# Kernel optimization log

Hardware: AMD Instinct MI355X
Metric: run time of the kernel (lower is better)

Reference implementation:

```python
import jax, jax.numpy as jnp
import numpy as np

C = 16      # internal_channel
DG = 8      # deform groups
KK = 9      # 3x3 kernel


def conv2d(x, w, b, pad):
    out = jax.lax.conv_general_dilated(
        x, w, (1, 1), [(pad, pad), (pad, pad)],
        dimension_numbers=('NCHW', 'OIHW', 'NCHW'))
    return out + b[None, :, None, None]


def feature_extraction(img, w1, b1, w2, b2, w3, b3):
    f1 = jax.nn.relu(conv2d(img, w1, b1, 1))   # [B,C,H,W]
    f2 = jax.nn.relu(conv2d(f1, w2, b2, 0))    # [B,C,H-2,W-2]
    f3 = jax.nn.relu(conv2d(f2, w3, b3, 0))    # [B,C,H-4,W-4]
    return [f1, f2, f3]


def deform_conv(x, offset, w, b):
    # x: [B,C,H,W]; offset: [B, DG*KK*2, H, W] (y,x pairs); w: [Cout,C,3,3]
    B, Cin, H, W = x.shape
    Cg = Cin // DG
    off = offset.reshape(B, DG, KK, 2, H, W)
    ky = jnp.repeat(jnp.arange(3) - 1, 3)  # kernel y offsets (pad=1)
    kx = jnp.tile(jnp.arange(3) - 1, 3)
    base_y = jnp.arange(H).reshape(1, 1, 1, H, 1)
    base_x = jnp.arange(W).reshape(1, 1, 1, 1, W)
    sy = base_y + ky.reshape(1, 1, KK, 1, 1) + off[:, :, :, 0]  # [B,DG,KK,H,W]
    sx = base_x + kx.reshape(1, 1, KK, 1, 1) + off[:, :, :, 1]
    y0 = jnp.floor(sy)
    x0 = jnp.floor(sx)
    wy = (sy - y0)[:, :, None]  # [B,DG,1,KK,H,W]
    wx = (sx - x0)[:, :, None]
    y0i = y0.astype(jnp.int32)
    x0i = x0.astype(jnp.int32)
    xg = x.reshape(B, DG, Cg, H * W)

    def gather(yy, xx):
        valid = (yy >= 0) & (yy < H) & (xx >= 0) & (xx < W)  # zero pad outside
        idx = (jnp.clip(yy, 0, H - 1) * W + jnp.clip(xx, 0, W - 1))
        idx_b = jnp.broadcast_to(idx.reshape(B, DG, 1, KK, H * W), (B, DG, Cg, KK, H * W))
        src = jnp.broadcast_to(xg[:, :, :, None, :], (B, DG, Cg, KK, H * W))
        g = jnp.take_along_axis(src, idx_b, axis=-1).reshape(B, DG, Cg, KK, H, W)
        return g * valid[:, :, None].astype(x.dtype)

    v00 = gather(y0i, x0i)
    v01 = gather(y0i, x0i + 1)
    v10 = gather(y0i + 1, x0i)
    v11 = gather(y0i + 1, x0i + 1)
    s = (v00 * (1 - wy) * (1 - wx) + v01 * (1 - wy) * wx
         + v10 * wy * (1 - wx) + v11 * wy * wx)
    s = s.reshape(B, Cin, KK, H, W)
    out = jnp.einsum('bckhw,ock->bohw', s, w.reshape(w.shape[0], Cin, KK))
    return out + b[None, :, None, None]


def setup_inputs() -> dict:
    key = jax.random.key(0)
    ks = jax.random.split(key, 24)
    B, H, W = 4, 192, 192
    sc = 0.05
    d = {
        'ref_image': jax.random.normal(ks[0], (B, C, H, W), jnp.float32),
        'unreg_image': jax.random.normal(ks[1], (B, C, H, W), jnp.float32),
        'fe_w1': jax.random.normal(ks[2], (C, C, 3, 3), jnp.float32) * sc,
        'fe_b1': jnp.zeros((C,), jnp.float32),
        'fe_w2': jax.random.normal(ks[3], (C, C, 3, 3), jnp.float32) * sc,
        'fe_b2': jnp.zeros((C,), jnp.float32),
        'fe_w3': jax.random.normal(ks[4], (C, C, 3, 3), jnp.float32) * sc,
        'fe_b3': jnp.zeros((C,), jnp.float32),
        'off_w0': jax.random.normal(ks[5], (C, 2 * C, 3, 3), jnp.float32) * sc,
        'off_b0': jnp.zeros((C,), jnp.float32),
        'off_w1': jax.random.normal(ks[6], (C, 2 * C, 3, 3), jnp.float32) * sc,
        'off_b1': jnp.zeros((C,), jnp.float32),
        'off_w2': jax.random.normal(ks[7], (C, 2 * C, 3, 3), jnp.float32) * sc,
        'off_b2': jnp.zeros((C,), jnp.float32),
        'dcn_off_w': jax.random.normal(ks[8], (2 * DG * KK, C, 3, 3), jnp.float32) * sc,
        'dcn_off_b': jnp.zeros((2 * DG * KK,), jnp.float32),
        'dcn_w': jax.random.normal(ks[9], (C, C, 3, 3), jnp.float32) * sc,
        'dcn_b': jnp.zeros((C,), jnp.float32),
    }
    return d


def reference(ref_image, unreg_image, fe_w1, fe_b1, fe_w2, fe_b2, fe_w3, fe_b3,
              off_w0, off_b0, off_w1, off_b1, off_w2, off_b2,
              dcn_off_w, dcn_off_b, dcn_w, dcn_b):
    ref_f = feature_extraction(ref_image, fe_w1, fe_b1, fe_w2, fe_b2, fe_w3, fe_b3)
    unr_f = feature_extraction(unreg_image, fe_w1, fe_b1, fe_w2, fe_b2, fe_w3, fe_b3)
    off_ws = [(off_w0, off_b0), (off_w1, off_b1), (off_w2, off_b2)]
    aligned = [None, None, None]
    for i in range(2, -1, -1):  # coarse-to-fine as in the source loop
        cat = jnp.concatenate([ref_f[i], unr_f[i]], axis=1)        # [B,2C,h,w]
        off_feat = jax.nn.relu(conv2d(cat, off_ws[i][0], off_ws[i][1], 1))
        offsets = conv2d(off_feat, dcn_off_w, dcn_off_b, 1)        # [B,2*DG*KK,h,w]
        aligned[i] = deform_conv(unr_f[i], offsets, dcn_w, dcn_b)
    return tuple(aligned)
```

## Files before the change

kernel.cpp:

```cpp
#include <hip/hip_runtime.h>

typedef unsigned int uint;
typedef unsigned short ushort;
typedef __attribute__((ext_vector_type(8))) short bf16x8;
typedef __attribute__((ext_vector_type(4))) float f32x4;

__device__ inline ushort f2bf(float f) {
    uint u = __float_as_uint(f);
    u += 0x7fff + ((u >> 16) & 1);
    return (ushort)(u >> 16);
}
__device__ inline float bflo(uint w) { return __uint_as_float(w << 16); }
__device__ inline float bfhi(uint w) { return __uint_as_float(w & 0xffff0000u); }

__global__ void packall_k(
    const float* __restrict__ fe_w1, const float* __restrict__ fe_w2,
    const float* __restrict__ fe_w3, const float* __restrict__ off_w0,
    const float* __restrict__ off_w1, const float* __restrict__ off_w2,
    const float* __restrict__ dcn_off_w, const float* __restrict__ dcn_w,
    ushort* __restrict__ pf1, ushort* __restrict__ pf2, ushort* __restrict__ pf3,
    ushort* __restrict__ po0, ushort* __restrict__ po1, ushort* __restrict__ po2,
    ushort* __restrict__ pow_, ushort* __restrict__ pd) {
    const int y = blockIdx.y;
    int i = blockIdx.x * 256 + threadIdx.x;
    const float* w; ushort* pk; int CIN, NT, KS;
    switch (y) {
        case 0: w = fe_w1;  pk = pf1;  CIN = 16; NT = 1; KS = 5; break;
        case 1: w = fe_w2;  pk = pf2;  CIN = 16; NT = 1; KS = 5; break;
        case 2: w = fe_w3;  pk = pf3;  CIN = 16; NT = 1; KS = 5; break;
        case 3: w = off_w0; pk = po0;  CIN = 32; NT = 1; KS = 9; break;
        case 4: w = off_w1; pk = po1;  CIN = 32; NT = 1; KS = 9; break;
        case 5: w = off_w2; pk = po2;  CIN = 32; NT = 1; KS = 9; break;
        case 6: w = dcn_off_w; pk = pow_; CIN = 16; NT = 9; KS = 5; break;
        default: w = dcn_w; pk = pd;   CIN = 16; NT = 1; KS = 5; break;
    }
    if (i >= KS * NT * 512) return;
    int e = i & 7, lane = (i >> 3) & 63, rest = i >> 9;
    int nt = rest % NT, ks = rest / NT;
    int k = ks * 32 + (lane >> 4) * 8 + e;
    int n = nt * 16 + (lane & 15);
    int t, ci;
    if (CIN == 16) { t = k >> 4; ci = k & 15; } else { t = k >> 5; ci = k & 31; }
    float v = (t < 9) ? w[(n * CIN + ci) * 9 + t] : 0.f;
    pk[i] = f2bf(v);
}

template <bool PLANAR>
__launch_bounds__(256)
__global__ void fe_mfma_k(const float* __restrict__ pA, const float* __restrict__ pB,
                          const ushort* __restrict__ catin,
                          const ushort* __restrict__ pack, const float* __restrict__ bias,
                          ushort* __restrict__ catout,
                          int H, int W, int OH, int OW, int pad) {
    __shared__ ushort patch[324 * 16];
    const int tid = threadIdx.x;
    const int tx0 = blockIdx.x * 16, ty0 = blockIdx.y * 16;
    const int b = blockIdx.z & 3, img = blockIdx.z >> 2;
    const int bx = tx0 - pad, by = ty0 - pad;
    const int HW = H * W;

    if (PLANAR) {
        const float* inb = (img ? pB : pA) + (size_t)(b * 16) * HW;
        for (int pos = tid; pos < 324; pos += 256) {
            int r = pos / 18, c = pos - r * 18;
            int gy = by + r, gx = bx + c;
            bool ok = (unsigned)gy < (unsigned)H && (unsigned)gx < (unsigned)W;
            int base = gy * W + gx;
            uint o16[8];
#pragma unroll
            for (int ii = 0; ii < 8; ++ii) {
                float lo = ok ? inb[(2 * ii) * HW + base] : 0.f;
                float hi = ok ? inb[(2 * ii + 1) * HW + base] : 0.f;
                o16[ii] = (uint)f2bf(lo) | ((uint)f2bf(hi) << 16);
            }
            *(uint4*)(patch + pos * 16) = *(uint4*)&o16[0];
            *(uint4*)(patch + pos * 16 + 8) = *(uint4*)&o16[4];
        }
    } else {
        for (int c = tid; c < 648; c += 256) {
            int pos = c >> 1, h = c & 1;
            int r = pos / 18, col = pos - r * 18;
            int gy = by + r, gx = bx + col;
            uint4 v = make_uint4(0, 0, 0, 0);
            if ((unsigned)gy < (unsigned)H && (unsigned)gx < (unsigned)W)
                v = *(const uint4*)(catin + ((size_t)(b * H + gy) * W + gx) * 32 + img * 16 + h * 8);
            *(uint4*)(patch + pos * 16 + h * 8) = v;
        }
    }
    __syncthreads();

    const int lane = tid & 63, wv = tid >> 6;
    const int g = lane >> 4, ci0 = (g & 1) * 8, rowx = lane & 15;
    f32x4 acc[4];
    float bv = bias[rowx];
#pragma unroll
    for (int m = 0; m < 4; ++m) acc[m] = f32x4{bv, bv, bv, bv};

#pragma unroll
    for (int ks = 0; ks < 5; ++ks) {
        int t = 2 * ks + (g >> 1);
        int dy = t < 9 ? t / 3 : 0;
        int dx = t < 9 ? t - (t / 3) * 3 : 0;
        bf16x8 a[4];
#pragma unroll
        for (int m = 0; m < 4; ++m) {
            int r = wv * 4 + m + dy, cc = rowx + dx;
            a[m] = *(const bf16x8*)(patch + (r * 18 + cc) * 16 + ci0);
        }
        bf16x8 bfrag = *(const bf16x8*)((const uint4*)pack + ks * 64 + lane);
#pragma unroll
        for (int m = 0; m < 4; ++m)
            acc[m] = __builtin_amdgcn_mfma_f32_16x16x32_bf16(a[m], bfrag, acc[m], 0, 0, 0);
    }

    const int oxb = g * 4;
#pragma unroll
    for (int m = 0; m < 4; ++m) {
        int gy = ty0 + wv * 4 + m;
        if (gy >= OH) continue;
#pragma unroll
        for (int j = 0; j < 4; ++j) {
            int gx = tx0 + oxb + j;
            if (gx < OW)
                catout[((size_t)(b * OH + gy) * OW + gx) * 32 + img * 16 + rowx] =
                    f2bf(fmaxf(acc[m][j], 0.f));
        }
    }
}

__launch_bounds__(256)
__global__ void off_mfma_k(const ushort* __restrict__ c0, const ushort* __restrict__ c1,
                           const ushort* __restrict__ c2,
                           const ushort* __restrict__ pk0, const ushort* __restrict__ pk1,
                           const ushort* __restrict__ pk2,
                           const float* __restrict__ b0, const float* __restrict__ b1,
                           const float* __restrict__ b2,
                           ushort* __restrict__ f0, ushort* __restrict__ f1,
                           ushort* __restrict__ f2) {
    const int z = blockIdx.z, s = z >> 2, b = z & 3;
    const int H = 192 - 2 * s, W = H;
    const ushort* cat  = s == 0 ? c0 : (s == 1 ? c1 : c2);
    const ushort* pack = s == 0 ? pk0 : (s == 1 ? pk1 : pk2);
    const float* bias  = s == 0 ? b0 : (s == 1 ? b1 : b2);
    ushort* out        = s == 0 ? f0 : (s == 1 ? f1 : f2);

    __shared__ ushort patch[324 * 32];
    const int tid = threadIdx.x;
    const int tx0 = blockIdx.x * 16, ty0 = blockIdx.y * 16;
    const int bx = tx0 - 1, by = ty0 - 1;

    for (int c = tid; c < 1296; c += 256) {
        int pos = c >> 2, h = c & 3;
        int r = pos / 18, col = pos - r * 18;
        int gy = by + r, gx = bx + col;
        uint4 v = make_uint4(0, 0, 0, 0);
        if ((unsigned)gy < (unsigned)H && (unsigned)gx < (unsigned)W)
            v = *(const uint4*)(cat + ((size_t)(b * H + gy) * W + gx) * 32 + h * 8);
        *(uint4*)(patch + pos * 32 + h * 8) = v;
    }
    __syncthreads();

    const int lane = tid & 63, wv = tid >> 6;
    const int g = lane >> 4, ci0 = g * 8, rowx = lane & 15;
    f32x4 acc[4];
    float bv = bias[rowx];
#pragma unroll
    for (int m = 0; m < 4; ++m) acc[m] = f32x4{bv, bv, bv, bv};

#pragma unroll
    for (int ks = 0; ks < 9; ++ks) {
        int dy = ks / 3, dx = ks - (ks / 3) * 3;
        bf16x8 a[4];
#pragma unroll
        for (int m = 0; m < 4; ++m) {
            int r = wv * 4 + m + dy, cc = rowx + dx;
            a[m] = *(const bf16x8*)(patch + (r * 18 + cc) * 32 + ci0);
        }
        bf16x8 bfrag = *(const bf16x8*)((const uint4*)pack + ks * 64 + lane);
#pragma unroll
        for (int m = 0; m < 4; ++m)
            acc[m] = __builtin_amdgcn_mfma_f32_16x16x32_bf16(a[m], bfrag, acc[m], 0, 0, 0);
    }

    const int oxb = g * 4;
#pragma unroll
    for (int m = 0; m < 4; ++m) {
        int gy = ty0 + wv * 4 + m;
        if (gy >= H) continue;
#pragma unroll
        for (int j = 0; j < 4; ++j) {
            int gx = tx0 + oxb + j;
            if (gx < W)
                out[((size_t)(b * H + gy) * W + gx) * 16 + rowx] = f2bf(fmaxf(acc[m][j], 0.f));
        }
    }
}

__launch_bounds__(256)
__global__ void dcn_fused_k(const ushort* __restrict__ c0, const ushort* __restrict__ c1,
                            const ushort* __restrict__ c2,
                            const ushort* __restrict__ fb0, const ushort* __restrict__ fb1,
                            const ushort* __restrict__ fb2,
                            const ushort* __restrict__ owPack, const float* __restrict__ ob,
                            const ushort* __restrict__ pd, const float* __restrict__ db,
                            float* __restrict__ o0, float* __restrict__ o1,
                            float* __restrict__ o2) {
    const int z = blockIdx.z;
    const int s = z >> 2, b = z & 3;
    const int H = 192 - 2 * s, W = H;
    const ushort* cat = s == 0 ? c0 : (s == 1 ? c1 : c2);
    const ushort* fb  = s == 0 ? fb0 : (s == 1 ? fb1 : fb2);
    float* out        = s == 0 ? o0 : (s == 1 ? o1 : o2);
    const int HW = H * W;
    const size_t pixb = (size_t)b * HW;

    __shared__ uint   xtu[8 * 484];
    __shared__ ushort ot[4 * 16 * 152];

    const int tid = threadIdx.x;
    const int tx0 = blockIdx.x * 16, ty0 = blockIdx.y * 16;

    {
        const int bx3 = tx0 - 3, by3 = ty0 - 3;
        for (int pos = tid; pos < 484; pos += 256) {
            int r = pos / 22, c = pos - r * 22;
            int gy2 = by3 + r, gx2 = bx3 + c;
            uint4 va = make_uint4(0, 0, 0, 0), vb = va;
            if ((unsigned)gy2 < (unsigned)H && (unsigned)gx2 < (unsigned)W) {
                const ushort* src = cat + (pixb + gy2 * W + gx2) * 32 + 16;
                va = *(const uint4*)src;
                vb = *(const uint4*)(src + 8);
            }
            xtu[0 * 484 + pos] = va.x; xtu[1 * 484 + pos] = va.y;
            xtu[2 * 484 + pos] = va.z; xtu[3 * 484 + pos] = va.w;
            xtu[4 * 484 + pos] = vb.x; xtu[5 * 484 + pos] = vb.y;
            xtu[6 * 484 + pos] = vb.z; xtu[7 * 484 + pos] = vb.w;
        }
    }
    __syncthreads();

    const int lane = tid & 63, wv = tid >> 6;
    const int g = lane >> 4, rowx = lane & 15, half = g & 1;
    const int ci0 = half * 8;
    const int px = tx0 + rowx;
    const float bv2 = db[rowx];
    ushort* otw = ot + wv * (16 * 152);

#pragma unroll 1
    for (int m = 0; m < 4; ++m) {
        const int py = ty0 + wv * 4 + m;

        f32x4 acc[9];
#pragma unroll
        for (int n = 0; n < 9; ++n) {
            float bv = ob[n * 16 + rowx];
            acc[n] = f32x4{bv, bv, bv, bv};
        }
#pragma unroll 1
        for (int ks = 0; ks < 5; ++ks) {
            int t = 2 * ks + (g >> 1);
            int dy = t < 9 ? t / 3 : 0;
            int dx = t < 9 ? t - (t / 3) * 3 : 0;
            int gya = ty0 - 1 + wv * 4 + m + dy;
            int gxa = tx0 - 1 + rowx + dx;
            uint4 av4 = make_uint4(0, 0, 0, 0);
            if ((unsigned)gya < (unsigned)H && (unsigned)gxa < (unsigned)W)
                av4 = *(const uint4*)(fb + ((size_t)(b * H + gya) * W + gxa) * 16 + ci0);
            bf16x8 a = *(bf16x8*)&av4;
            const uint4* bp = (const uint4*)owPack + (size_t)(ks * 9) * 64 + lane;
#pragma unroll
            for (int n = 0; n < 9; ++n) {
                bf16x8 bfrag = *(const bf16x8*)(bp + (size_t)n * 64);
                acc[n] = __builtin_amdgcn_mfma_f32_16x16x32_bf16(a, bfrag, acc[n], 0, 0, 0);
            }
        }

#pragma unroll
        for (int n = 0; n < 9; ++n) {
            int ch = n * 16 + rowx;
            int dg = ch / 18;
            int rem = ch - dg * 18;
            int col = (rem >> 1) * 16 + dg * 2 + (rem & 1);
#pragma unroll
            for (int j = 0; j < 4; ++j)
                otw[(g * 4 + j) * 152 + col] = f2bf(acc[n][j]);
        }

        f32x4 acc2 = f32x4{bv2, bv2, bv2, bv2};
#pragma unroll 1
        for (int ks = 0; ks < 5; ++ks) {
            const int t = 2 * ks + (g >> 1);
            const bool tv = (t < 9);
            const int t3 = t / 3;
            const int ky = (tv ? t3 : 0) - 1, kx = (tv ? t - t3 * 3 : 0) - 1;

            uint a2[4];
            if (tv) {
                uint4 ov = *(const uint4*)(otw + rowx * 152 + t * 16 + half * 8);
                uint ovv[4] = {ov.x, ov.y, ov.z, ov.w};
#pragma unroll
                for (int d = 0; d < 4; ++d) {
                    const int dgA = half * 4 + d;
                    uint u = ovv[d];
                    float sy = (float)(py + ky) + bflo(u);
                    float sx = (float)(px + kx) + bfhi(u);
                    float fy = floorf(sy), fx = floorf(sx);
                    int y0 = (int)fy, x0 = (int)fx;
                    float wy = sy - fy, wx = sx - fx;
                    float wy1 = 1.f - wy, wx1 = 1.f - wx;
                    float w00 = wy1 * wx1, w01 = wy1 * wx, w10 = wy * wx1, w11 = wy * wx;
                    int ly = y0 - (ty0 - 3), lx = x0 - (tx0 - 3);
                    float2 v00, v01, v10, v11;
                    if ((unsigned)ly <= 20u && (unsigned)lx <= 20u) {
                        const uint* tt = &xtu[dgA * 484 + ly * 22 + lx];
                        uint u00 = tt[0], u01 = tt[1], u10 = tt[22], u11 = tt[23];
                        v00 = make_float2(bflo(u00), bfhi(u00));
                        v01 = make_float2(bflo(u01), bfhi(u01));
                        v10 = make_float2(bflo(u10), bfhi(u10));
                        v11 = make_float2(bflo(u11), bfhi(u11));
                    } else {
                        v00 = v01 = v10 = v11 = make_float2(0.f, 0.f);
                        bool y0v = (unsigned)y0 < (unsigned)H;
                        bool y1v = (unsigned)(y0 + 1) < (unsigned)H;
                        bool x0v = (unsigned)x0 < (unsigned)W;
                        bool x1v = (unsigned)(x0 + 1) < (unsigned)W;
                        const ushort* cg = cat + ((size_t)pixb + (size_t)y0 * W + x0) * 32 + 16 + 2 * dgA;
                        if (y0v && x0v) { uint uu = *(const uint*)cg;                 v00 = make_float2(bflo(uu), bfhi(uu)); }
                        if (y0v && x1v) { uint uu = *(const uint*)(cg + 32);          v01 = make_float2(bflo(uu), bfhi(uu)); }
                        if (y1v && x0v) { uint uu = *(const uint*)(cg + 32 * W);      v10 = make_float2(bflo(uu), bfhi(uu)); }
                        if (y1v && x1v) { uint uu = *(const uint*)(cg + 32 * W + 32); v11 = make_float2(bflo(uu), bfhi(uu)); }
                    }
                    float s0 = w00 * v00.x + w01 * v01.x + w10 * v10.x + w11 * v11.x;
                    float s1 = w00 * v00.y + w01 * v01.y + w10 * v10.y + w11 * v11.y;
                    a2[d] = (uint)f2bf(s0) | ((uint)f2bf(s1) << 16);
                }
            } else {
                a2[0] = a2[1] = a2[2] = a2[3] = 0u;
            }
            uint4 av = make_uint4(a2[0], a2[1], a2[2], a2[3]);
            bf16x8 af = *(bf16x8*)&av;
            bf16x8 dfrag = *(const bf16x8*)((const uint4*)pd + ks * 64 + lane);
            acc2 = __builtin_amdgcn_mfma_f32_16x16x32_bf16(af, dfrag, acc2, 0, 0, 0);
        }

        if (py < H) {
            float* op = out + (size_t)(b * 16 + rowx) * HW + (size_t)py * W;
#pragma unroll
            for (int j = 0; j < 4; ++j) {
                int gx2 = tx0 + g * 4 + j;
                if (gx2 < W) op[gx2] = acc2[j];
            }
        }
    }
}

extern "C" void kernel_launch(void* const* d_in, const int* in_sizes, int n_in,
                              void* d_out, int out_size, void* d_ws, size_t ws_size,
                              hipStream_t stream) {
    const float* ref_image = (const float*)d_in[0];
    const float* unreg_image = (const float*)d_in[1];
    const float* fe_w1 = (const float*)d_in[2];
    const float* fe_b1 = (const float*)d_in[3];
    const float* fe_w2 = (const float*)d_in[4];
    const float* fe_b2 = (const float*)d_in[5];
    const float* fe_w3 = (const float*)d_in[6];
    const float* fe_b3 = (const float*)d_in[7];
    const float* off_w0 = (const float*)d_in[8];
    const float* off_b0 = (const float*)d_in[9];
    const float* off_w1 = (const float*)d_in[10];
    const float* off_b1 = (const float*)d_in[11];
    const float* off_w2 = (const float*)d_in[12];
    const float* off_b2 = (const float*)d_in[13];
    const float* dcn_off_w = (const float*)d_in[14];
    const float* dcn_off_b = (const float*)d_in[15];
    const float* dcn_w = (const float*)d_in[16];
    const float* dcn_b = (const float*)d_in[17];

    const size_t pix[3] = {4ul * 192 * 192, 4ul * 190 * 190, 4ul * 188 * 188};
    const size_t szf[3] = {pix[0] * 16, pix[1] * 16, pix[2] * 16};

    size_t o = 0;
    auto take = [&](size_t bytes) {
        void* r = (char*)d_ws + o;
        o += (bytes + 255) & ~(size_t)255;
        return r;
    };
    ushort* cat[3]; ushort* fb[3];
    ushort* pf[3]; ushort* po[3]; ushort* owPack; ushort* pd;
    for (int s = 0; s < 3; ++s) cat[s] = (ushort*)take(pix[s] * 32 * 2);
    for (int s = 0; s < 3; ++s) fb[s] = (ushort*)take(pix[s] * 16 * 2);
    for (int s = 0; s < 3; ++s) pf[s] = (ushort*)take(2560 * 2);
    for (int s = 0; s < 3; ++s) po[s] = (ushort*)take(4608 * 2);
    owPack = (ushort*)take(23040 * 2);
    pd = (ushort*)take(2560 * 2);

    float* out0 = (float*)d_out;
    float* out1 = out0 + szf[0];
    float* out2 = out1 + szf[1];

    dim3 blk(256);

    packall_k<<<dim3(90, 8), blk, 0, stream>>>(
        fe_w1, fe_w2, fe_w3, off_w0, off_w1, off_w2, dcn_off_w, dcn_w,
        pf[0], pf[1], pf[2], po[0], po[1], po[2], owPack, pd);

    fe_mfma_k<true><<<dim3(12, 12, 8), blk, 0, stream>>>(
        ref_image, unreg_image, nullptr, pf[0], fe_b1, cat[0], 192, 192, 192, 192, 1);
    fe_mfma_k<false><<<dim3(12, 12, 8), blk, 0, stream>>>(
        nullptr, nullptr, cat[0], pf[1], fe_b2, cat[1], 192, 192, 190, 190, 0);
    fe_mfma_k<false><<<dim3(12, 12, 8), blk, 0, stream>>>(
        nullptr, nullptr, cat[1], pf[2], fe_b3, cat[2], 190, 190, 188, 188, 0);

    off_mfma_k<<<dim3(12, 12, 12), blk, 0, stream>>>(
        cat[0], cat[1], cat[2], po[0], po[1], po[2],
        off_b0, off_b1, off_b2, fb[0], fb[1], fb[2]);

    dcn_fused_k<<<dim3(12, 12, 12), blk, 0, stream>>>(
        cat[0], cat[1], cat[2], fb[0], fb[1], fb[2],
        owPack, dcn_off_b, pd, dcn_b, out0, out1, out2);
}
```

Baseline: 172.3 us.

## Keep DCN offsets in MFMA accumulators, dropping the LDS round-trip

The offset-conv MFMA is transposed so weights become the A operand, with the packed weight rows permuted. Each lane's accumulator then directly holds the (dy,dx) offsets it needs for the bilinear sampling, so the bf16 store to LDS and the reload are gone. The DCN weight pack is permuted to match the new K ordering. The change also software-prefetches the next feature fragment, fully unrolls the sampling loop and packs results with v_cvt_pk_bf16_f32. Offsets now stay in fp32 instead of being rounded to bf16, which shifts numerics slightly, and register pressure rises with the full unroll.

```diff
diff --git a/kernel.cpp b/kernel.cpp
--- a/kernel.cpp
+++ b/kernel.cpp
@@ -9,6 +9,11 @@
     uint u = __float_as_uint(f);
     u += 0x7fff + ((u >> 16) & 1);
     return (ushort)(u >> 16);
+}
+__device__ inline uint pkbf(float lo, float hi) {
+    uint r;
+    asm("v_cvt_pk_bf16_f32 %0, %1, %2" : "=v"(r) : "v"(lo), "v"(hi));
+    return r;
 }
 __device__ inline float bflo(uint w) { return __uint_as_float(w << 16); }
 __device__ inline float bfhi(uint w) { return __uint_as_float(w & 0xffff0000u); }
@@ -23,22 +28,43 @@
     ushort* __restrict__ pow_, ushort* __restrict__ pd) {
     const int y = blockIdx.y;
     int i = blockIdx.x * 256 + threadIdx.x;
-    const float* w; ushort* pk; int CIN, NT, KS;
+    int e = i & 7, lane = (i >> 3) & 63, rest = i >> 9;
+    if (y == 6) {
+        if (i >= 23040) return;
+        int nt = rest % 9, ks = rest / 9;
+        int m_idx = lane & 15;
+        int ghat = m_idx >> 2, rhat = m_idx & 3;
+        int c_orig = (2 * ghat + (rhat >> 1)) * 18 + nt * 2 + (rhat & 1);
+        int k = ks * 32 + (lane >> 4) * 8 + e;
+        int tapk = k >> 4, ci = k & 15;
+        float v = (tapk < 9) ? dcn_off_w[(c_orig * 16 + ci) * 9 + tapk] : 0.f;
+        pow_[i] = f2bf(v);
+        return;
+    }
+    if (y == 7) {
+        if (i >= 2560) return;
+        int ks = rest;
+        int co = lane & 15;
+        int tap = 2 * ks + (e >> 2);
+        int dg = 2 * (lane >> 4) + ((e >> 1) & 1);
+        int ci = dg * 2 + (e & 1);
+        float v = (tap < 9) ? dcn_w[(co * 16 + ci) * 9 + tap] : 0.f;
+        pd[i] = f2bf(v);
+        return;
+    }
+    const float* w; ushort* pk; int CIN, KS;
     switch (y) {
-        case 0: w = fe_w1;  pk = pf1;  CIN = 16; NT = 1; KS = 5; break;
-        case 1: w = fe_w2;  pk = pf2;  CIN = 16; NT = 1; KS = 5; break;
-        case 2: w = fe_w3;  pk = pf3;  CIN = 16; NT = 1; KS = 5; break;
-        case 3: w = off_w0; pk = po0;  CIN = 32; NT = 1; KS = 9; break;
-        case 4: w = off_w1; pk = po1;  CIN = 32; NT = 1; KS = 9; break;
-        case 5: w = off_w2; pk = po2;  CIN = 32; NT = 1; KS = 9; break;
-        case 6: w = dcn_off_w; pk = pow_; CIN = 16; NT = 9; KS = 5; break;
-        default: w = dcn_w; pk = pd;   CIN = 16; NT = 1; KS = 5; break;
-    }
-    if (i >= KS * NT * 512) return;
-    int e = i & 7, lane = (i >> 3) & 63, rest = i >> 9;
-    int nt = rest % NT, ks = rest / NT;
+        case 0: w = fe_w1;  pk = pf1;  CIN = 16; KS = 5; break;
+        case 1: w = fe_w2;  pk = pf2;  CIN = 16; KS = 5; break;
+        case 2: w = fe_w3;  pk = pf3;  CIN = 16; KS = 5; break;
+        case 3: w = off_w0; pk = po0;  CIN = 32; KS = 9; break;
+        case 4: w = off_w1; pk = po1;  CIN = 32; KS = 9; break;
+        default: w = off_w2; pk = po2; CIN = 32; KS = 9; break;
+    }
+    if (i >= KS * 512) return;
+    int ks = rest;
     int k = ks * 32 + (lane >> 4) * 8 + e;
-    int n = nt * 16 + (lane & 15);
+    int n = lane & 15;
     int t, ci;
     if (CIN == 16) { t = k >> 4; ci = k & 15; } else { t = k >> 5; ci = k & 31; }
     float v = (t < 9) ? w[(n * CIN + ci) * 9 + t] : 0.f;
@@ -214,8 +240,7 @@
     const int HW = H * W;
     const size_t pixb = (size_t)b * HW;
 
-    __shared__ uint   xtu[8 * 484];
-    __shared__ ushort ot[4 * 16 * 152];
+    __shared__ uint xtu[8 * 484];
 
     const int tid = threadIdx.x;
     const int tx0 = blockIdx.x * 16, ty0 = blockIdx.y * 16;
@@ -240,70 +265,63 @@
     __syncthreads();
 
     const int lane = tid & 63, wv = tid >> 6;
-    const int g = lane >> 4, rowx = lane & 15, half = g & 1;
-    const int ci0 = half * 8;
+    const int g = lane >> 4, rowx = lane & 15;
+    const int ci0 = (g & 1) * 8;
     const int px = tx0 + rowx;
     const float bv2 = db[rowx];
-    ushort* otw = ot + wv * (16 * 152);
 
 #pragma unroll 1
     for (int m = 0; m < 4; ++m) {
         const int py = ty0 + wv * 4 + m;
 
+        auto loadB = [&](int ks) -> uint4 {
+            int t = 2 * ks + (g >> 1);
+            int tc = t < 9 ? t : 0;
+            int dy = tc / 3, dx = tc - (tc / 3) * 3;
+            int gya = ty0 - 1 + wv * 4 + m + dy;
+            int gxa = tx0 - 1 + rowx + dx;
+            uint4 r = make_uint4(0, 0, 0, 0);
+            if ((unsigned)gya < (unsigned)H && (unsigned)gxa < (unsigned)W)
+                r = *(const uint4*)(fb + ((size_t)(b * H + gya) * W + gxa) * 16 + ci0);
+            return r;
+        };
+
         f32x4 acc[9];
 #pragma unroll
         for (int n = 0; n < 9; ++n) {
-            float bv = ob[n * 16 + rowx];
-            acc[n] = f32x4{bv, bv, bv, bv};
-        }
+            f32x4 t;
+#pragma unroll
+            for (int r = 0; r < 4; ++r)
+                t[r] = ob[(2 * g + (r >> 1)) * 18 + n * 2 + (r & 1)];
+            acc[n] = t;
+        }
+        uint4 bvc = loadB(0);
 #pragma unroll 1
         for (int ks = 0; ks < 5; ++ks) {
-            int t = 2 * ks + (g >> 1);
-            int dy = t < 9 ? t / 3 : 0;
-            int dx = t < 9 ? t - (t / 3) * 3 : 0;
-            int gya = ty0 - 1 + wv * 4 + m + dy;
-            int gxa = tx0 - 1 + rowx + dx;
-            uint4 av4 = make_uint4(0, 0, 0, 0);
-            if ((unsigned)gya < (unsigned)H && (unsigned)gxa < (unsigned)W)
-                av4 = *(const uint4*)(fb + ((size_t)(b * H + gya) * W + gxa) * 16 + ci0);
-            bf16x8 a = *(bf16x8*)&av4;
-            const uint4* bp = (const uint4*)owPack + (size_t)(ks * 9) * 64 + lane;
+            uint4 bvn = make_uint4(0, 0, 0, 0);
+            if (ks < 4) bvn = loadB(ks + 1);
+            bf16x8 bfrag = *(bf16x8*)&bvc;
+            const uint4* ap = (const uint4*)owPack + (size_t)(ks * 9) * 64 + lane;
 #pragma unroll
             for (int n = 0; n < 9; ++n) {
-                bf16x8 bfrag = *(const bf16x8*)(bp + (size_t)n * 64);
-                acc[n] = __builtin_amdgcn_mfma_f32_16x16x32_bf16(a, bfrag, acc[n], 0, 0, 0);
+                bf16x8 afrag = *(const bf16x8*)(ap + (size_t)n * 64);
+                acc[n] = __builtin_amdgcn_mfma_f32_16x16x32_bf16(afrag, bfrag, acc[n], 0, 0, 0);
             }
-        }
-
-#pragma unroll
-        for (int n = 0; n < 9; ++n) {
-            int ch = n * 16 + rowx;
-            int dg = ch / 18;
-            int rem = ch - dg * 18;
-            int col = (rem >> 1) * 16 + dg * 2 + (rem & 1);
-#pragma unroll
-            for (int j = 0; j < 4; ++j)
-                otw[(g * 4 + j) * 152 + col] = f2bf(acc[n][j]);
+            bvc = bvn;
         }
 
         f32x4 acc2 = f32x4{bv2, bv2, bv2, bv2};
-#pragma unroll 1
+#pragma unroll
         for (int ks = 0; ks < 5; ++ks) {
-            const int t = 2 * ks + (g >> 1);
-            const bool tv = (t < 9);
-            const int t3 = t / 3;
-            const int ky = (tv ? t3 : 0) - 1, kx = (tv ? t - t3 * 3 : 0) - 1;
-
             uint a2[4];
-            if (tv) {
-                uint4 ov = *(const uint4*)(otw + rowx * 152 + t * 16 + half * 8);
-                uint ovv[4] = {ov.x, ov.y, ov.z, ov.w};
-#pragma unroll
-                for (int d = 0; d < 4; ++d) {
-                    const int dgA = half * 4 + d;
-                    uint u = ovv[d];
-                    float sy = (float)(py + ky) + bflo(u);
-                    float sx = (float)(px + kx) + bfhi(u);
+#pragma unroll
+            for (int u = 0; u < 4; ++u) {
+                const int tap = 2 * ks + (u >> 1);
+                if (tap < 9) {
+                    const int dgA = 2 * g + (u & 1);
+                    const int ky = tap / 3 - 1, kx = tap % 3 - 1;
+                    float sy = (float)(py + ky) + acc[tap][(u & 1) * 2];
+                    float sx = (float)(px + kx) + acc[tap][(u & 1) * 2 + 1];
                     float fy = floorf(sy), fx = floorf(sx);
                     int y0 = (int)fy, x0 = (int)fx;
                     float wy = sy - fy, wx = sx - fx;
@@ -324,7 +342,7 @@
                         bool y1v = (unsigned)(y0 + 1) < (unsigned)H;
                         bool x0v = (unsigned)x0 < (unsigned)W;
                         bool x1v = (unsigned)(x0 + 1) < (unsigned)W;
-                        const ushort* cg = cat + ((size_t)pixb + (size_t)y0 * W + x0) * 32 + 16 + 2 * dgA;
+                        const ushort* cg = cat + (pixb + (size_t)y0 * W + x0) * 32 + 16 + 2 * dgA;
                         if (y0v && x0v) { uint uu = *(const uint*)cg;                 v00 = make_float2(bflo(uu), bfhi(uu)); }
                         if (y0v && x1v) { uint uu = *(const uint*)(cg + 32);          v01 = make_float2(bflo(uu), bfhi(uu)); }
                         if (y1v && x0v) { uint uu = *(const uint*)(cg + 32 * W);      v10 = make_float2(bflo(uu), bfhi(uu)); }
@@ -332,10 +350,10 @@
                     }
                     float s0 = w00 * v00.x + w01 * v01.x + w10 * v10.x + w11 * v11.x;
                     float s1 = w00 * v00.y + w01 * v01.y + w10 * v10.y + w11 * v11.y;
-                    a2[d] = (uint)f2bf(s0) | ((uint)f2bf(s1) << 16);
+                    a2[u] = pkbf(s0, s1);
+                } else {
+                    a2[u] = 0u;
                 }
-            } else {
-                a2[0] = a2[1] = a2[2] = a2[3] = 0u;
             }
             uint4 av = make_uint4(a2[0], a2[1], a2[2], a2[3]);
             bf16x8 af = *(bf16x8*)&av;
```

Result: faster. 160.1 us, median of 2 (-7.0%).
